# Kernel tuning notes

Measured on AMD Instinct MI355X. Metric: run time of the kernel, lower is better.

The kernel has to match this reference:

```python
import jax, jax.numpy as jnp
import numpy as np

D = 512  # token_dim == hidden_dim
K = 65536  # number of trajectory tokens


def safe_normalize(v, eps=1e-6):
    n = jnp.linalg.norm(v, axis=-1, keepdims=True)
    ok = n > eps
    e1 = jnp.zeros_like(v).at[..., 0].set(1.0)
    return jnp.where(ok, v / jnp.maximum(n, eps), e1)


def rot6d_to_matrix(x, eps=1e-6):
    # x: (K, 6) -> R: (K, 3, 3), rows (a1, b2, a3)
    a1 = safe_normalize(x[..., 0:3], eps)
    a2 = x[..., 3:6]
    proj = jnp.sum(a1 * a2, axis=-1, keepdims=True) * a1
    b2 = safe_normalize(a2 - proj, eps)
    a3 = safe_normalize(jnp.cross(a1, b2), eps)
    b2 = safe_normalize(jnp.cross(a3, a1), eps)
    return jnp.stack((a1, b2, a3), axis=-2)


def geodesic_angle(R_pred, R_gt, eps=1e-8):
    # RtR = R_gt^T @ R_pred, per-element (K,3,3)
    RtR = jnp.einsum('kji,kjl->kil', R_gt, R_pred)
    trace = RtR[..., 0, 0] + RtR[..., 1, 1] + RtR[..., 2, 2]
    c = jnp.clip((trace - 1.0) * 0.5, -1.0 + 1e-6, 1.0 - 1e-6)
    skew = RtR - jnp.swapaxes(RtR, -1, -2)
    v = jnp.stack([skew[..., 2, 1], skew[..., 0, 2], skew[..., 1, 0]], axis=-1)
    s = 0.5 * jnp.linalg.norm(v, axis=-1) + eps
    return jnp.arctan2(s, c)


def huber(pred, target, beta, mask):
    # smooth-L1 with beta, masked mean (denominator = clamped mask sum)
    d = jnp.abs(pred - target)
    l = jnp.where(d < beta, 0.5 * d * d / beta, d - 0.5 * beta) * mask
    return l.sum() / jnp.maximum(mask.sum(), 1.0)


def rot_loss_fn(pred, gt):
    # pred, gt: (K, 12) = [L rot6d(6), R rot6d(6)]
    Lp, Rp = pred[:, :6], pred[:, 6:]
    Lt, Rt = gt[:, :6], gt[:, 6:]
    Lvalid = jnp.all(Lt != -1000.0, axis=-1)
    Rvalid = jnp.all(Rt != -1000.0, axis=-1)
    safe6 = jnp.array([1.0, 0.0, 0.0, 0.0, 1.0, 0.0], pred.dtype)
    Lt = jnp.where(Lvalid[:, None], Lt, safe6)
    Rt = jnp.where(Rvalid[:, None], Rt, safe6)
    ang_L = geodesic_angle(rot6d_to_matrix(Lp), rot6d_to_matrix(Lt))
    ang_R = geodesic_angle(rot6d_to_matrix(Rp), rot6d_to_matrix(Rt))
    wL = Lvalid.astype(pred.dtype)
    wR = Rvalid.astype(pred.dtype)
    denom = jnp.maximum(wL.sum() + wR.sum(), 1e-8)
    num = jnp.sum(wL * jnp.where(Lvalid, ang_L, 0.0)) + jnp.sum(wR * jnp.where(Rvalid, ang_R, 0.0))
    return num / denom


def _heads(hidden_states, w1, b1, w2, b2, w3, b3):
    # 4 stacked MLPs (m = time, coord, coord2d, quat), torch Linear layout (out, in)
    h1 = jax.nn.relu(jnp.einsum('kc,mhc->mkh', hidden_states, w1) + b1[:, None, :])
    h2 = jax.nn.relu(jnp.einsum('mkh,mgh->mkg', h1, w2) + b2[:, None, :])
    pred_time = h2[0] @ w3[0:1].T + b3[0:1]      # (K, 1)
    pred_coords = h2[1] @ w3[1:7].T + b3[1:7]    # (K, 6)
    pred_2d = h2[2] @ w3[7:11].T + b3[7:11]      # (K, 4)
    pred_quat = h2[3] @ w3[11:23].T + b3[11:23]  # (K, 12)
    return pred_time, pred_coords, pred_2d, pred_quat


def _loss(pred_time, pred_coords, pred_2d, pred_quat, gt,
          beta_3d=0.07, beta_2d=0.02, beta_time=3.0, sigma_time=3.0):
    time_gt = gt[:, 0:1]
    time_valid = (time_gt != -1000.0).astype(jnp.float32)
    xyz_gt = gt[:, 1:7]
    xyz_valid = (xyz_gt != -1000.0).astype(jnp.float32)
    uv_gt = gt[:, 7:11]
    uv_valid = (uv_gt != -1000.0).astype(jnp.float32)
    quat_gt = gt[:, 11:23]
    quat_valid = (quat_gt != -1000.0).astype(jnp.float32)

    time_loss = huber(pred_time, time_gt, beta_time, time_valid)

    dt = jnp.abs(pred_time - time_gt)
    w_t = jnp.where(time_valid.sum() > 0,
                    jnp.exp(-0.5 * (dt / sigma_time) ** 2) * time_valid,
                    jnp.ones_like(pred_time))  # (K, 1), broadcasts over feature dims

    loss_3d = huber(pred_coords, xyz_gt, beta_3d, xyz_valid * w_t)
    loss_2d = huber(pred_2d / 1408.0, uv_gt / 1408.0, beta_2d, uv_valid * w_t)
    quat_huber = huber(pred_quat, quat_gt, 0.2, quat_valid * w_t)
    rot_l = 0.15 * rot_loss_fn(pred_quat, quat_gt)

    return 1.0 * time_loss + 2.0 * loss_3d + 0.5 * loss_2d + 0.5 * quat_huber + rot_l


def setup_inputs() -> dict:
    key = jax.random.key(0)
    ks = jax.random.split(key, 6)
    s = 1.0 / np.sqrt(D)
    return {
        'hidden_states': jax.random.normal(ks[0], (K, D), jnp.float32),
        'gt_traj': jax.random.uniform(ks[1], (K, 23), jnp.float32),
        'w1': jax.random.normal(ks[2], (4, D, D), jnp.float32) * s,
        'b1': jnp.zeros((4, D), jnp.float32),
        'w2': jax.random.normal(ks[3], (4, D, D), jnp.float32) * s,
        'b2': jnp.zeros((4, D), jnp.float32),
        'w3': jax.random.normal(ks[4], (23, D), jnp.float32) * s,
        'b3': jnp.zeros((23,), jnp.float32),
    }


def reference(hidden_states, gt_traj, w1, b1, w2, b2, w3, b3):
    pred_time, pred_coords, pred_2d, pred_quat = _heads(hidden_states, w1, b1, w2, b2, w3, b3)
    total_loss = _loss(pred_time, pred_coords, pred_2d, pred_quat, gt_traj)
    packed = jnp.concatenate(
        [pred_coords.reshape(-1, 2, 3), pred_quat.reshape(-1, 2, 6)], axis=-1
    ).reshape(-1, 18)
    return pred_time, packed, total_loss
```

## Files before the change

kernel.cpp:

```cpp
#include <hip/hip_runtime.h>
#include <math.h>


#define KROWS 65536
#define DH 512

typedef _Float16 f16;
typedef _Float16 half8 __attribute__((ext_vector_type(8)));
typedef float floatx4 __attribute__((ext_vector_type(4)));

#define WS_WF16   0
#define WS_W3F16  4194304
#define WS_PRED2D 4227072
#define WS_PART   5275648

__global__ __launch_bounds__(256) void convert_weights(
    const float* __restrict__ w1, const float* __restrict__ w2,
    const float* __restrict__ w3, f16* __restrict__ wf16, f16* __restrict__ w3f16)
{
  int t = blockIdx.x * 256 + threadIdx.x;
  if (t < 262144) {
    int ml = t >> 15;
    int mm = ml >> 1, l = ml & 1;
    int r = t & 32767;
    int fb = r >> 6;
    int lane = r & 63;
    int nt = fb >> 4, kq = fb & 15;
    int n = nt * 16 + (lane & 15);
    int k = kq * 32 + (lane >> 4) * 8;
    const float* src = (l ? w2 : w1) + (size_t)mm * 262144 + n * 512 + k;
    floatx4 u0 = *(const floatx4*)(src);
    floatx4 u1 = *(const floatx4*)(src + 4);
    half8 h;
    h[0] = (f16)u0[0]; h[1] = (f16)u0[1]; h[2] = (f16)u0[2]; h[3] = (f16)u0[3];
    h[4] = (f16)u1[0]; h[5] = (f16)u1[1]; h[6] = (f16)u1[2]; h[7] = (f16)u1[3];
    *(half8*)(wf16 + (size_t)ml * 262144 + fb * 512 + lane * 8) = h;
  } else {
    int j = t - 262144;
    if (j < 23 * DH) w3f16[j] = (f16)w3[j];
  }
}

extern __shared__ unsigned char smem[];

__global__ __launch_bounds__(512, 2) void fused_kernel(
    const float* __restrict__ hidden,
    const f16* __restrict__ wf16,
    const f16* __restrict__ w3f16,
    const float* __restrict__ b1g,
    const float* __restrict__ b2g,
    const float* __restrict__ b3g,
    float* __restrict__ dout,
    float* __restrict__ pred2d)
{
  const int r0  = blockIdx.x * 64;
  const int tid = threadIdx.x;
  const int w   = __builtin_amdgcn_readfirstlane(tid >> 6);
  const int lane = tid & 63;
  const int l15 = lane & 15;
  const int lg  = lane >> 4;

  unsigned char* Ab = smem;
  unsigned char* hb = smem + 65536;

  const int arow = l15 * 128;
  const int ao   = (lg * 16) ^ ((l15 & 7) << 4);
  auto aread = [&](const unsigned char* chunk, int mt, int kq) -> half8 {
    return *(const half8*)(chunk + mt * 2048 + arow + (ao ^ (kq << 6)));
  };
  const f16* bptr = wf16 + lane * 8;
  auto bload = [&](int mm, int l, int g, int nt) -> half8 {
    return *(const half8*)(bptr + ((mm * 2 + l)) * 262144
                           + ((w * 4 + nt) * 16 + g) * 512);
  };

  {
    const int row = tid >> 3;
    const int cg  = tid & 7;
    const int sw  = ((cg * 16) ^ ((row & 7) << 4));
    const float* hr = hidden + (size_t)(r0 + row) * DH + cg * 8;
    unsigned char* dst = Ab + row * 128 + sw;
#pragma unroll
    for (int kc = 0; kc < 8; ++kc) {
      floatx4 u0 = *(const floatx4*)(hr + kc * 64);
      floatx4 u1 = *(const floatx4*)(hr + kc * 64 + 4);
      half8 p;
      p[0] = (f16)u0[0]; p[1] = (f16)u0[1]; p[2] = (f16)u0[2]; p[3] = (f16)u0[3];
      p[4] = (f16)u1[0]; p[5] = (f16)u1[1]; p[6] = (f16)u1[2]; p[7] = (f16)u1[3];
      *(half8*)(dst + kc * 8192) = p;
    }
  }

  floatx4 acc[4][4];
  const floatx4 zf = {0.f, 0.f, 0.f, 0.f};
  const half8 hz = {(f16)0, (f16)0, (f16)0, (f16)0, (f16)0, (f16)0, (f16)0, (f16)0};

  __syncthreads();

#pragma unroll 1
  for (int m = 0; m < 4; ++m) {
#pragma unroll
    for (int mt = 0; mt < 4; ++mt)
#pragma unroll
      for (int nt = 0; nt < 4; ++nt) acc[mt][nt] = zf;

    half8 c0 = bload(m, 0, 0, 0), c1 = bload(m, 0, 0, 1),
          c2 = bload(m, 0, 0, 2), c3 = bload(m, 0, 0, 3);
#pragma unroll 1
    for (int g = 0; g < 16; ++g) {
      half8 n0, n1, n2, n3;
      if (g < 15) {
        n0 = bload(m, 0, g + 1, 0); n1 = bload(m, 0, g + 1, 1);
        n2 = bload(m, 0, g + 1, 2); n3 = bload(m, 0, g + 1, 3);
      }
      const unsigned char* chunk = Ab + (g >> 1) * 8192;
#pragma unroll
      for (int mt = 0; mt < 4; ++mt) {
        half8 a = aread(chunk, mt, g & 1);
        acc[mt][0] = __builtin_amdgcn_mfma_f32_16x16x32_f16(a, c0, acc[mt][0], 0, 0, 0);
        acc[mt][1] = __builtin_amdgcn_mfma_f32_16x16x32_f16(a, c1, acc[mt][1], 0, 0, 0);
        acc[mt][2] = __builtin_amdgcn_mfma_f32_16x16x32_f16(a, c2, acc[mt][2], 0, 0, 0);
        acc[mt][3] = __builtin_amdgcn_mfma_f32_16x16x32_f16(a, c3, acc[mt][3], 0, 0, 0);
      }
      c0 = n0; c1 = n1; c2 = n2; c3 = n3;
    }

    {
      unsigned char* myc = hb + w * 8192;
#pragma unroll
      for (int nt = 0; nt < 4; ++nt) {
        const float bv = b1g[m * DH + w * 64 + nt * 16 + l15];
        const int cb = 2 * (nt * 16 + l15);
#pragma unroll
        for (int mt = 0; mt < 4; ++mt)
#pragma unroll
          for (int j = 0; j < 4; ++j) {
            float v = fmaxf(acc[mt][nt][j] + bv, 0.f);
            int row = mt * 16 + 4 * lg + j;
            *(f16*)(myc + row * 128 + (cb ^ ((row & 7) << 4))) = (f16)v;
          }
      }
    }
    __syncthreads();

#pragma unroll
    for (int mt = 0; mt < 4; ++mt)
#pragma unroll
      for (int nt = 0; nt < 4; ++nt) acc[mt][nt] = zf;

    c0 = bload(m, 1, 0, 0); c1 = bload(m, 1, 0, 1);
    c2 = bload(m, 1, 0, 2); c3 = bload(m, 1, 0, 3);
#pragma unroll 1
    for (int g = 0; g < 16; ++g) {
      half8 n0, n1, n2, n3;
      if (g < 15) {
        n0 = bload(m, 1, g + 1, 0); n1 = bload(m, 1, g + 1, 1);
        n2 = bload(m, 1, g + 1, 2); n3 = bload(m, 1, g + 1, 3);
      }
      const unsigned char* chunk = hb + (g >> 1) * 8192;
#pragma unroll
      for (int mt = 0; mt < 4; ++mt) {
        half8 a = aread(chunk, mt, g & 1);
        acc[mt][0] = __builtin_amdgcn_mfma_f32_16x16x32_f16(a, c0, acc[mt][0], 0, 0, 0);
        acc[mt][1] = __builtin_amdgcn_mfma_f32_16x16x32_f16(a, c1, acc[mt][1], 0, 0, 0);
        acc[mt][2] = __builtin_amdgcn_mfma_f32_16x16x32_f16(a, c2, acc[mt][2], 0, 0, 0);
        acc[mt][3] = __builtin_amdgcn_mfma_f32_16x16x32_f16(a, c3, acc[mt][3], 0, 0, 0);
      }
      c0 = n0; c1 = n1; c2 = n2; c3 = n3;
    }
    __syncthreads();

    {
      unsigned char* myc = hb + w * 8192;
#pragma unroll
      for (int nt = 0; nt < 4; ++nt) {
        const float bv = b2g[m * DH + w * 64 + nt * 16 + l15];
        const int cb = 2 * (nt * 16 + l15);
#pragma unroll
        for (int mt = 0; mt < 4; ++mt)
#pragma unroll
          for (int j = 0; j < 4; ++j) {
            float v = fmaxf(acc[mt][nt][j] + bv, 0.f);
            int row = mt * 16 + 4 * lg + j;
            *(f16*)(myc + row * 128 + (cb ^ ((row & 7) << 4))) = (f16)v;
          }
      }
    }
    __syncthreads();

    if (w < 4) {
      const int base_m = (m == 0) ? 0 : (m == 1) ? 1 : (m == 2) ? 7 : 11;
      const int cnt_m  = (m == 0) ? 1 : (m == 1) ? 6 : (m == 2) ? 4 : 12;
      const bool ovalid = l15 < cnt_m;
      const f16* w3row = w3f16 + (size_t)(base_m + (ovalid ? l15 : 0)) * DH;
      floatx4 acc3 = zf;
#pragma unroll
      for (int q = 0; q < 16; ++q) {
        half8 ah = aread(hb + (q >> 1) * 8192, w, q & 1);
        half8 wv = ovalid ? *(const half8*)(w3row + q * 32 + lg * 8) : hz;
        acc3 = __builtin_amdgcn_mfma_f32_16x16x32_f16(ah, wv, acc3, 0, 0, 0);
      }
      if (ovalid) {
        const float bo = b3g[base_m + l15];
#pragma unroll
        for (int j = 0; j < 4; ++j) {
          const int row = r0 + w * 16 + 4 * lg + j;
          const float v = acc3[j] + bo;
          if (m == 0)      { if (l15 == 0) dout[row] = v; }
          else if (m == 1) { dout[KROWS + row * 18 + (l15 < 3 ? l15 : l15 + 6)] = v; }
          else if (m == 2) { pred2d[row * 4 + l15] = v; }
          else             { dout[KROWS + row * 18 + (l15 < 6 ? l15 + 3 : l15 + 6)] = v; }
        }
      }
    }
    __syncthreads();
  }
}

__device__ __forceinline__ void safe_norm3(float x, float y, float z, float* o) {
  float n = sqrtf(x * x + y * y + z * z);
  if (n > 1e-6f) { o[0] = x / n; o[1] = y / n; o[2] = z / n; }
  else           { o[0] = 1.f;   o[1] = 0.f;   o[2] = 0.f; }
}

__device__ __forceinline__ void rot6d(const float* x, float* R) {
  float a1[3]; safe_norm3(x[0], x[1], x[2], a1);
  float d = a1[0] * x[3] + a1[1] * x[4] + a1[2] * x[5];
  float b2[3]; safe_norm3(x[3] - d * a1[0], x[4] - d * a1[1], x[5] - d * a1[2], b2);
  float a3[3];
  safe_norm3(a1[1] * b2[2] - a1[2] * b2[1],
             a1[2] * b2[0] - a1[0] * b2[2],
             a1[0] * b2[1] - a1[1] * b2[0], a3);
  float bb[3];
  safe_norm3(a3[1] * a1[2] - a3[2] * a1[1],
             a3[2] * a1[0] - a3[0] * a1[2],
             a3[0] * a1[1] - a3[1] * a1[0], bb);
  R[0] = a1[0]; R[1] = a1[1]; R[2] = a1[2];
  R[3] = bb[0]; R[4] = bb[1]; R[5] = bb[2];
  R[6] = a3[0]; R[7] = a3[1]; R[8] = a3[2];
}

__device__ __forceinline__ float geo_angle(const float* P, const float* G) {
  float M[9];
#pragma unroll
  for (int i = 0; i < 3; ++i)
#pragma unroll
    for (int l = 0; l < 3; ++l)
      M[i * 3 + l] = G[0 + i] * P[0 + l] + G[3 + i] * P[3 + l] + G[6 + i] * P[6 + l];
  float tr = M[0] + M[4] + M[8];
  float c = fminf(fmaxf((tr - 1.f) * 0.5f, -1.f + 1e-6f), 1.f - 1e-6f);
  float v0 = M[7] - M[5], v1 = M[2] - M[6], v2 = M[3] - M[1];
  float s = 0.5f * sqrtf(v0 * v0 + v1 * v1 + v2 * v2) + 1e-8f;
  return atan2f(s, c);
}

__global__ __launch_bounds__(256) void loss_partial(
    const float* __restrict__ gt, const float* __restrict__ dout,
    const float* __restrict__ pred2d, float* __restrict__ partials)
{
  const int r = blockIdx.x * 256 + threadIdx.x;
  const float* g  = gt + (size_t)r * 23;
  const float* pk = dout + KROWS + (size_t)r * 18;
  float a[17];

  const float pt = dout[r];
  const float tg = g[0];
  const float tv = (tg != -1000.f) ? 1.f : 0.f;
  const float dt = fabsf(pt - tg);
  a[0] = ((dt < 3.f) ? (0.5f * dt * dt / 3.f) : (dt - 1.5f)) * tv;
  a[1] = tv;
  a[2] = tv;
  const float wt = expf(-0.5f * (dt / 3.f) * (dt / 3.f)) * tv;

  float n3T = 0.f, d3T = 0.f, n3F = 0.f, d3F = 0.f;
#pragma unroll
  for (int j = 0; j < 6; ++j) {
    const float p = pk[j < 3 ? j : j + 6];
    const float q = g[1 + j];
    const float val = (q != -1000.f) ? 1.f : 0.f;
    const float d = fabsf(p - q);
    const float l = (d < 0.07f) ? (0.5f * d * d / 0.07f) : (d - 0.035f);
    n3T += l * val * wt; d3T += val * wt; n3F += l * val; d3F += val;
  }
  a[3] = n3T; a[4] = d3T; a[5] = n3F; a[6] = d3F;

  float n2T = 0.f, d2T = 0.f, n2F = 0.f, d2F = 0.f;
#pragma unroll
  for (int j = 0; j < 4; ++j) {
    const float p = pred2d[(size_t)r * 4 + j];
    const float q = g[7 + j];
    const float val = (q != -1000.f) ? 1.f : 0.f;
    const float d = fabsf(p / 1408.f - q / 1408.f);
    const float l = (d < 0.02f) ? (0.5f * d * d / 0.02f) : (d - 0.01f);
    n2T += l * val * wt; d2T += val * wt; n2F += l * val; d2F += val;
  }
  a[7] = n2T; a[8] = d2T; a[9] = n2F; a[10] = d2F;

  float qp[12];
#pragma unroll
  for (int j = 0; j < 12; ++j) qp[j] = pk[j < 6 ? j + 3 : j + 6];
  float nqT = 0.f, dqT = 0.f, nqF = 0.f, dqF = 0.f;
#pragma unroll
  for (int j = 0; j < 12; ++j) {
    const float q = g[11 + j];
    const float val = (q != -1000.f) ? 1.f : 0.f;
    const float d = fabsf(qp[j] - q);
    const float l = (d < 0.2f) ? (0.5f * d * d / 0.2f) : (d - 0.1f);
    nqT += l * val * wt; dqT += val * wt; nqF += l * val; dqF += val;
  }
  a[11] = nqT; a[12] = dqT; a[13] = nqF; a[14] = dqF;

  bool Lv = true, Rv = true;
#pragma unroll
  for (int j = 0; j < 6; ++j) {
    if (g[11 + j] == -1000.f) Lv = false;
    if (g[17 + j] == -1000.f) Rv = false;
  }
  const float safe6[6] = {1.f, 0.f, 0.f, 0.f, 1.f, 0.f};
  float Lt[6], Rt[6];
#pragma unroll
  for (int j = 0; j < 6; ++j) {
    Lt[j] = Lv ? g[11 + j] : safe6[j];
    Rt[j] = Rv ? g[17 + j] : safe6[j];
  }
  float Rp[9], Rg[9];
  rot6d(qp, Rp);     rot6d(Lt, Rg);
  const float angL = geo_angle(Rp, Rg);
  rot6d(qp + 6, Rp); rot6d(Rt, Rg);
  const float angR = geo_angle(Rp, Rg);
  a[15] = (Lv ? angL : 0.f) + (Rv ? angR : 0.f);
  a[16] = (Lv ? 1.f : 0.f) + (Rv ? 1.f : 0.f);

#pragma unroll
  for (int i = 0; i < 17; ++i) {
    float v = a[i];
#pragma unroll
    for (int off = 32; off > 0; off >>= 1) v += __shfl_down(v, off, 64);
    a[i] = v;
  }
  __shared__ float red[4][17];
  if ((threadIdx.x & 63) == 0) {
    const int wv = threadIdx.x >> 6;
#pragma unroll
    for (int i = 0; i < 17; ++i) red[wv][i] = a[i];
  }
  __syncthreads();
  if (threadIdx.x < 17)
    partials[blockIdx.x * 20 + threadIdx.x] =
        red[0][threadIdx.x] + red[1][threadIdx.x] + red[2][threadIdx.x] + red[3][threadIdx.x];
}

__global__ void loss_final(const float* __restrict__ partials, float* __restrict__ dout)
{
  __shared__ float s[17];
  const int i = threadIdx.x;
  if (i < 17) {
    float v = 0.f;
    for (int b = 0; b < 256; ++b) v += partials[b * 20 + i];
    s[i] = v;
  }
  __syncthreads();
  if (i == 0) {
    const bool flag = s[2] > 0.f;
    const float time_loss = s[0] / fmaxf(s[1], 1.f);
    const float l3 = flag ? s[3] / fmaxf(s[4], 1.f) : s[5] / fmaxf(s[6], 1.f);
    const float l2 = flag ? s[7] / fmaxf(s[8], 1.f) : s[9] / fmaxf(s[10], 1.f);
    const float lq = flag ? s[11] / fmaxf(s[12], 1.f) : s[13] / fmaxf(s[14], 1.f);
    const float rot = 0.15f * (s[15] / fmaxf(s[16], 1e-8f));
    dout[19 * KROWS] = time_loss + 2.f * l3 + 0.5f * l2 + 0.5f * lq + rot;
  }
}

extern "C" void kernel_launch(void* const* d_in, const int* in_sizes, int n_in,
                              void* d_out, int out_size, void* d_ws, size_t ws_size,
                              hipStream_t stream) {
  (void)in_sizes; (void)n_in; (void)out_size; (void)ws_size;
  const float* hidden = (const float*)d_in[0];
  const float* gt     = (const float*)d_in[1];
  const float* w1     = (const float*)d_in[2];
  const float* b1     = (const float*)d_in[3];
  const float* w2     = (const float*)d_in[4];
  const float* b2     = (const float*)d_in[5];
  const float* w3     = (const float*)d_in[6];
  const float* b3     = (const float*)d_in[7];
  float* dout = (float*)d_out;

  unsigned char* ws = (unsigned char*)d_ws;
  f16*   wf16     = (f16*)(ws + WS_WF16);
  f16*   w3f16    = (f16*)(ws + WS_W3F16);
  float* pred2d   = (float*)(ws + WS_PRED2D);
  float* partials = (float*)(ws + WS_PART);

  static bool attr_done = false;
  if (!attr_done) {
    hipFuncSetAttribute(reinterpret_cast<const void*>(fused_kernel),
                        hipFuncAttributeMaxDynamicSharedMemorySize, 131072);
    attr_done = true;
  }

  convert_weights<<<1070, 256, 0, stream>>>(w1, w2, w3, wf16, w3f16);
  fused_kernel<<<1024, 512, 131072, stream>>>(hidden, wf16, w3f16, b1, b2, b3, dout, pred2d);
  loss_partial<<<256, 256, 0, stream>>>(gt, dout, pred2d, partials);
  loss_final<<<1, 64, 0, stream>>>(partials, dout);
}
```

Baseline: 370.6 us.

## Split fused MLP blocks into 32-row tiles and two head-pairs per block

Each block now handles 32 rows and only two of the four MLP heads, selected by block parity, so the grid grows to 4096 blocks. Shared memory per block drops to 64 KB and launch bounds request 4 blocks per CU, aiming for higher occupancy and better latency hiding. The cost is that every hidden row is loaded and converted twice, and each weight fragment feeds half as many MFMAs (2 row tiles instead of 4), which raises weight traffic per FLOP. A sync after the layer-1 GEMM replaces the end-of-loop sync so the layer-1 epilogue cannot overwrite hb while the previous head's output projection is still reading it.

```diff
diff --git a/kernel.cpp b/kernel.cpp
--- a/kernel.cpp
+++ b/kernel.cpp
@@ -43,7 +43,7 @@
 
 extern __shared__ unsigned char smem[];
 
-__global__ __launch_bounds__(512, 2) void fused_kernel(
+__global__ __launch_bounds__(512, 4) void fused_kernel(
     const float* __restrict__ hidden,
     const f16* __restrict__ wf16,
     const f16* __restrict__ w3f16,
@@ -53,7 +53,10 @@
     float* __restrict__ dout,
     float* __restrict__ pred2d)
 {
-  const int r0  = blockIdx.x * 64;
+  const int bid = blockIdx.x;
+  const int hp  = bid & 1;
+  const int row_tile = bid >> 1;
+  const int r0  = row_tile * 32;
   const int tid = threadIdx.x;
   const int w   = __builtin_amdgcn_readfirstlane(tid >> 6);
   const int lane = tid & 63;
@@ -61,12 +64,13 @@
   const int lg  = lane >> 4;
 
   unsigned char* Ab = smem;
-  unsigned char* hb = smem + 65536;
+  unsigned char* hb = smem + 32768;
 
   const int arow = l15 * 128;
   const int ao   = (lg * 16) ^ ((l15 & 7) << 4);
-  auto aread = [&](const unsigned char* chunk, int mt, int kq) -> half8 {
-    return *(const half8*)(chunk + mt * 2048 + arow + (ao ^ (kq << 6)));
+  auto aread = [&](const unsigned char* base, int g, int mt) -> half8 {
+    return *(const half8*)(base + (g >> 1) * 4096 + mt * 2048 + arow
+                           + (ao ^ ((g & 1) << 6)));
   };
   const f16* bptr = wf16 + lane * 8;
   auto bload = [&](int mm, int l, int g, int nt) -> half8 {
@@ -75,64 +79,69 @@
   };
 
   {
-    const int row = tid >> 3;
-    const int cg  = tid & 7;
-    const int sw  = ((cg * 16) ^ ((row & 7) << 4));
-    const float* hr = hidden + (size_t)(r0 + row) * DH + cg * 8;
-    unsigned char* dst = Ab + row * 128 + sw;
-#pragma unroll
-    for (int kc = 0; kc < 8; ++kc) {
-      floatx4 u0 = *(const floatx4*)(hr + kc * 64);
-      floatx4 u1 = *(const floatx4*)(hr + kc * 64 + 4);
-      half8 p;
-      p[0] = (f16)u0[0]; p[1] = (f16)u0[1]; p[2] = (f16)u0[2]; p[3] = (f16)u0[3];
-      p[4] = (f16)u1[0]; p[5] = (f16)u1[1]; p[6] = (f16)u1[2]; p[7] = (f16)u1[3];
-      *(half8*)(dst + kc * 8192) = p;
-    }
-  }
-
-  floatx4 acc[4][4];
+    const int row = tid >> 4;
+    const int cg  = tid & 15;
+    const float* hr = hidden + (size_t)(r0 + row) * DH;
+#pragma unroll
+    for (int p = 0; p < 4; ++p) {
+      const int col = p * 128 + cg * 8;
+      const int kc  = col >> 6;
+      const int cic = col & 63;
+      floatx4 u0 = *(const floatx4*)(hr + col);
+      floatx4 u1 = *(const floatx4*)(hr + col + 4);
+      half8 pk;
+      pk[0] = (f16)u0[0]; pk[1] = (f16)u0[1]; pk[2] = (f16)u0[2]; pk[3] = (f16)u0[3];
+      pk[4] = (f16)u1[0]; pk[5] = (f16)u1[1]; pk[6] = (f16)u1[2]; pk[7] = (f16)u1[3];
+      *(half8*)(Ab + kc * 4096 + row * 128 + ((2 * cic) ^ ((row & 7) << 4))) = pk;
+    }
+  }
+
+  floatx4 acc[2][4];
   const floatx4 zf = {0.f, 0.f, 0.f, 0.f};
   const half8 hz = {(f16)0, (f16)0, (f16)0, (f16)0, (f16)0, (f16)0, (f16)0, (f16)0};
 
   __syncthreads();
 
 #pragma unroll 1
-  for (int m = 0; m < 4; ++m) {
-#pragma unroll
-    for (int mt = 0; mt < 4; ++mt)
+  for (int mi = 0; mi < 2; ++mi) {
+    const int m = hp * 2 + mi;
+#pragma unroll
+    for (int mt = 0; mt < 2; ++mt)
 #pragma unroll
       for (int nt = 0; nt < 4; ++nt) acc[mt][nt] = zf;
 
-    half8 c0 = bload(m, 0, 0, 0), c1 = bload(m, 0, 0, 1),
-          c2 = bload(m, 0, 0, 2), c3 = bload(m, 0, 0, 3);
+    {
+      half8 c0 = bload(m, 0, 0, 0), c1 = bload(m, 0, 0, 1),
+            c2 = bload(m, 0, 0, 2), c3 = bload(m, 0, 0, 3);
 #pragma unroll 1
-    for (int g = 0; g < 16; ++g) {
-      half8 n0, n1, n2, n3;
-      if (g < 15) {
-        n0 = bload(m, 0, g + 1, 0); n1 = bload(m, 0, g + 1, 1);
-        n2 = bload(m, 0, g + 1, 2); n3 = bload(m, 0, g + 1, 3);
-      }
-      const unsigned char* chunk = Ab + (g >> 1) * 8192;
-#pragma unroll
-      for (int mt = 0; mt < 4; ++mt) {
-        half8 a = aread(chunk, mt, g & 1);
-        acc[mt][0] = __builtin_amdgcn_mfma_f32_16x16x32_f16(a, c0, acc[mt][0], 0, 0, 0);
-        acc[mt][1] = __builtin_amdgcn_mfma_f32_16x16x32_f16(a, c1, acc[mt][1], 0, 0, 0);
-        acc[mt][2] = __builtin_amdgcn_mfma_f32_16x16x32_f16(a, c2, acc[mt][2], 0, 0, 0);
-        acc[mt][3] = __builtin_amdgcn_mfma_f32_16x16x32_f16(a, c3, acc[mt][3], 0, 0, 0);
-      }
-      c0 = n0; c1 = n1; c2 = n2; c3 = n3;
-    }
+      for (int g = 0; g < 16; ++g) {
+        half8 n0, n1, n2, n3;
+        if (g < 15) {
+          n0 = bload(m, 0, g + 1, 0); n1 = bload(m, 0, g + 1, 1);
+          n2 = bload(m, 0, g + 1, 2); n3 = bload(m, 0, g + 1, 3);
+        }
+#pragma unroll
+        for (int mt = 0; mt < 2; ++mt) {
+          half8 a = aread(Ab, g, mt);
+          acc[mt][0] = __builtin_amdgcn_mfma_f32_16x16x32_f16(a, c0, acc[mt][0], 0, 0, 0);
+          acc[mt][1] = __builtin_amdgcn_mfma_f32_16x16x32_f16(a, c1, acc[mt][1], 0, 0, 0);
+          acc[mt][2] = __builtin_amdgcn_mfma_f32_16x16x32_f16(a, c2, acc[mt][2], 0, 0, 0);
+          acc[mt][3] = __builtin_amdgcn_mfma_f32_16x16x32_f16(a, c3, acc[mt][3], 0, 0, 0);
+        }
+        c0 = n0; c1 = n1; c2 = n2; c3 = n3;
+      }
+    }
+
+    __syncthreads();
 
     {
-      unsigned char* myc = hb + w * 8192;
+      unsigned char* myc = hb + w * 4096;
 #pragma unroll
       for (int nt = 0; nt < 4; ++nt) {
         const float bv = b1g[m * DH + w * 64 + nt * 16 + l15];
         const int cb = 2 * (nt * 16 + l15);
 #pragma unroll
-        for (int mt = 0; mt < 4; ++mt)
+        for (int mt = 0; mt < 2; ++mt)
 #pragma unroll
           for (int j = 0; j < 4; ++j) {
             float v = fmaxf(acc[mt][nt][j] + bv, 0.f);
@@ -144,40 +153,41 @@
     __syncthreads();
 
 #pragma unroll
-    for (int mt = 0; mt < 4; ++mt)
+    for (int mt = 0; mt < 2; ++mt)
 #pragma unroll
       for (int nt = 0; nt < 4; ++nt) acc[mt][nt] = zf;
 
-    c0 = bload(m, 1, 0, 0); c1 = bload(m, 1, 0, 1);
-    c2 = bload(m, 1, 0, 2); c3 = bload(m, 1, 0, 3);
+    {
+      half8 c0 = bload(m, 1, 0, 0), c1 = bload(m, 1, 0, 1),
+            c2 = bload(m, 1, 0, 2), c3 = bload(m, 1, 0, 3);
 #pragma unroll 1
-    for (int g = 0; g < 16; ++g) {
-      half8 n0, n1, n2, n3;
-      if (g < 15) {
-        n0 = bload(m, 1, g + 1, 0); n1 = bload(m, 1, g + 1, 1);
-        n2 = bload(m, 1, g + 1, 2); n3 = bload(m, 1, g + 1, 3);
-      }
-      const unsigned char* chunk = hb + (g >> 1) * 8192;
-#pragma unroll
-      for (int mt = 0; mt < 4; ++mt) {
-        half8 a = aread(chunk, mt, g & 1);
-        acc[mt][0] = __builtin_amdgcn_mfma_f32_16x16x32_f16(a, c0, acc[mt][0], 0, 0, 0);
-        acc[mt][1] = __builtin_amdgcn_mfma_f32_16x16x32_f16(a, c1, acc[mt][1], 0, 0, 0);
-        acc[mt][2] = __builtin_amdgcn_mfma_f32_16x16x32_f16(a, c2, acc[mt][2], 0, 0, 0);
-        acc[mt][3] = __builtin_amdgcn_mfma_f32_16x16x32_f16(a, c3, acc[mt][3], 0, 0, 0);
-      }
-      c0 = n0; c1 = n1; c2 = n2; c3 = n3;
+      for (int g = 0; g < 16; ++g) {
+        half8 n0, n1, n2, n3;
+        if (g < 15) {
+          n0 = bload(m, 1, g + 1, 0); n1 = bload(m, 1, g + 1, 1);
+          n2 = bload(m, 1, g + 1, 2); n3 = bload(m, 1, g + 1, 3);
+        }
+#pragma unroll
+        for (int mt = 0; mt < 2; ++mt) {
+          half8 a = aread(hb, g, mt);
+          acc[mt][0] = __builtin_amdgcn_mfma_f32_16x16x32_f16(a, c0, acc[mt][0], 0, 0, 0);
+          acc[mt][1] = __builtin_amdgcn_mfma_f32_16x16x32_f16(a, c1, acc[mt][1], 0, 0, 0);
+          acc[mt][2] = __builtin_amdgcn_mfma_f32_16x16x32_f16(a, c2, acc[mt][2], 0, 0, 0);
+          acc[mt][3] = __builtin_amdgcn_mfma_f32_16x16x32_f16(a, c3, acc[mt][3], 0, 0, 0);
+        }
+        c0 = n0; c1 = n1; c2 = n2; c3 = n3;
+      }
     }
     __syncthreads();
 
     {
-      unsigned char* myc = hb + w * 8192;
+      unsigned char* myc = hb + w * 4096;
 #pragma unroll
       for (int nt = 0; nt < 4; ++nt) {
         const float bv = b2g[m * DH + w * 64 + nt * 16 + l15];
         const int cb = 2 * (nt * 16 + l15);
 #pragma unroll
-        for (int mt = 0; mt < 4; ++mt)
+        for (int mt = 0; mt < 2; ++mt)
 #pragma unroll
           for (int j = 0; j < 4; ++j) {
             float v = fmaxf(acc[mt][nt][j] + bv, 0.f);
@@ -188,15 +198,15 @@
     }
     __syncthreads();
 
-    if (w < 4) {
+    if (w < 2) {
       const int base_m = (m == 0) ? 0 : (m == 1) ? 1 : (m == 2) ? 7 : 11;
       const int cnt_m  = (m == 0) ? 1 : (m == 1) ? 6 : (m == 2) ? 4 : 12;
       const bool ovalid = l15 < cnt_m;
       const f16* w3row = w3f16 + (size_t)(base_m + (ovalid ? l15 : 0)) * DH;
       floatx4 acc3 = zf;
-#pragma unroll
+#pragma unroll 2
       for (int q = 0; q < 16; ++q) {
-        half8 ah = aread(hb + (q >> 1) * 8192, w, q & 1);
+        half8 ah = aread(hb, q, w);
         half8 wv = ovalid ? *(const half8*)(w3row + q * 32 + lg * 8) : hz;
         acc3 = __builtin_amdgcn_mfma_f32_16x16x32_f16(ah, wv, acc3, 0, 0, 0);
       }
@@ -213,7 +223,6 @@
         }
       }
     }
-    __syncthreads();
   }
 }
 
@@ -394,12 +403,12 @@
   static bool attr_done = false;
   if (!attr_done) {
     hipFuncSetAttribute(reinterpret_cast<const void*>(fused_kernel),
-                        hipFuncAttributeMaxDynamicSharedMemorySize, 131072);
+                        hipFuncAttributeMaxDynamicSharedMemorySize, 65536);
     attr_done = true;
   }
 
   convert_weights<<<1070, 256, 0, stream>>>(w1, w2, w3, wf16, w3f16);
-  fused_kernel<<<1024, 512, 131072, stream>>>(hidden, wf16, w3f16, b1, b2, b3, dout, pred2d);
+  fused_kernel<<<4096, 512, 65536, stream>>>(hidden, wf16, w3f16, b1, b2, b3, dout, pred2d);
   loss_partial<<<256, 256, 0, stream>>>(gt, dout, pred2d, partials);
   loss_final<<<1, 64, 0, stream>>>(partials, dout);
 }
```

New measurement: 458.1 us. 23.6% more time.

## Split the four MLP heads across blocks and reuse one shared buffer in place

Applied to the files above, without the earlier changes.

Each block now handles one head for one 64-row tile, so the grid grows from 1024 to 4096 blocks. Blocks with the same row tile are interleaved in launch order so they run close together. LDS per block drops from 128KB dynamic to 64KB static by writing hidden activations back over the input buffer. Launch bounds now request four waves per EU for higher occupancy. In exchange, each hidden tile is loaded and converted four times instead of once, and register pressure is tighter under the new occupancy target.

```diff
diff --git a/kernel.cpp b/kernel.cpp
--- a/kernel.cpp
+++ b/kernel.cpp
@@ -41,9 +41,9 @@
   }
 }
 
-extern __shared__ unsigned char smem[];
-
-__global__ __launch_bounds__(512, 2) void fused_kernel(
+__global__ __launch_bounds__(512, 4)
+__attribute__((amdgpu_waves_per_eu(4, 4)))
+void fused_kernel(
     const float* __restrict__ hidden,
     const f16* __restrict__ wf16,
     const f16* __restrict__ w3f16,
@@ -53,25 +53,28 @@
     float* __restrict__ dout,
     float* __restrict__ pred2d)
 {
-  const int r0  = blockIdx.x * 64;
+  __shared__ __align__(16) unsigned char smem[65536];
+
+  const int bid = blockIdx.x;
+  const int rr  = bid & 7;
+  const int m   = rr >> 1;
+  const int row_tile = ((bid >> 3) << 1) | (rr & 1);
+  const int r0  = row_tile * 64;
   const int tid = threadIdx.x;
   const int w   = __builtin_amdgcn_readfirstlane(tid >> 6);
   const int lane = tid & 63;
   const int l15 = lane & 15;
   const int lg  = lane >> 4;
 
-  unsigned char* Ab = smem;
-  unsigned char* hb = smem + 65536;
-
   const int arow = l15 * 128;
   const int ao   = (lg * 16) ^ ((l15 & 7) << 4);
-  auto aread = [&](const unsigned char* chunk, int mt, int kq) -> half8 {
-    return *(const half8*)(chunk + mt * 2048 + arow + (ao ^ (kq << 6)));
+  auto aread = [&](int g, int mt) -> half8 {
+    return *(const half8*)(smem + (g >> 1) * 8192 + mt * 2048 + arow
+                           + (ao ^ ((g & 1) << 6)));
   };
-  const f16* bptr = wf16 + lane * 8;
-  auto bload = [&](int mm, int l, int g, int nt) -> half8 {
-    return *(const half8*)(bptr + ((mm * 2 + l)) * 262144
-                           + ((w * 4 + nt) * 16 + g) * 512);
+  const f16* bptr = wf16 + (size_t)(m * 2) * 262144 + lane * 8;
+  auto bload = [&](int l, int g, int nt) -> half8 {
+    return *(const half8*)(bptr + l * 262144 + ((w * 4 + nt) * 16 + g) * 512);
   };
 
   {
@@ -79,7 +82,7 @@
     const int cg  = tid & 7;
     const int sw  = ((cg * 16) ^ ((row & 7) << 4));
     const float* hr = hidden + (size_t)(r0 + row) * DH + cg * 8;
-    unsigned char* dst = Ab + row * 128 + sw;
+    unsigned char* dst = smem + row * 128 + sw;
 #pragma unroll
     for (int kc = 0; kc < 8; ++kc) {
       floatx4 u0 = *(const floatx4*)(hr + kc * 64);
@@ -97,26 +100,24 @@
 
   __syncthreads();
 
-#pragma unroll 1
-  for (int m = 0; m < 4; ++m) {
-#pragma unroll
-    for (int mt = 0; mt < 4; ++mt)
-#pragma unroll
-      for (int nt = 0; nt < 4; ++nt) acc[mt][nt] = zf;
-
-    half8 c0 = bload(m, 0, 0, 0), c1 = bload(m, 0, 0, 1),
-          c2 = bload(m, 0, 0, 2), c3 = bload(m, 0, 0, 3);
+#pragma unroll
+  for (int mt = 0; mt < 4; ++mt)
+#pragma unroll
+    for (int nt = 0; nt < 4; ++nt) acc[mt][nt] = zf;
+
+  {
+    half8 c0 = bload(0, 0, 0), c1 = bload(0, 0, 1),
+          c2 = bload(0, 0, 2), c3 = bload(0, 0, 3);
 #pragma unroll 1
     for (int g = 0; g < 16; ++g) {
       half8 n0, n1, n2, n3;
       if (g < 15) {
-        n0 = bload(m, 0, g + 1, 0); n1 = bload(m, 0, g + 1, 1);
-        n2 = bload(m, 0, g + 1, 2); n3 = bload(m, 0, g + 1, 3);
+        n0 = bload(0, g + 1, 0); n1 = bload(0, g + 1, 1);
+        n2 = bload(0, g + 1, 2); n3 = bload(0, g + 1, 3);
       }
-      const unsigned char* chunk = Ab + (g >> 1) * 8192;
 #pragma unroll
       for (int mt = 0; mt < 4; ++mt) {
-        half8 a = aread(chunk, mt, g & 1);
+        half8 a = aread(g, mt);
         acc[mt][0] = __builtin_amdgcn_mfma_f32_16x16x32_f16(a, c0, acc[mt][0], 0, 0, 0);
         acc[mt][1] = __builtin_amdgcn_mfma_f32_16x16x32_f16(a, c1, acc[mt][1], 0, 0, 0);
         acc[mt][2] = __builtin_amdgcn_mfma_f32_16x16x32_f16(a, c2, acc[mt][2], 0, 0, 0);
@@ -124,43 +125,46 @@
       }
       c0 = n0; c1 = n1; c2 = n2; c3 = n3;
     }
-
-    {
-      unsigned char* myc = hb + w * 8192;
-#pragma unroll
-      for (int nt = 0; nt < 4; ++nt) {
-        const float bv = b1g[m * DH + w * 64 + nt * 16 + l15];
-        const int cb = 2 * (nt * 16 + l15);
-#pragma unroll
-        for (int mt = 0; mt < 4; ++mt)
-#pragma unroll
-          for (int j = 0; j < 4; ++j) {
-            float v = fmaxf(acc[mt][nt][j] + bv, 0.f);
-            int row = mt * 16 + 4 * lg + j;
-            *(f16*)(myc + row * 128 + (cb ^ ((row & 7) << 4))) = (f16)v;
-          }
-      }
-    }
-    __syncthreads();
-
-#pragma unroll
-    for (int mt = 0; mt < 4; ++mt)
-#pragma unroll
-      for (int nt = 0; nt < 4; ++nt) acc[mt][nt] = zf;
-
-    c0 = bload(m, 1, 0, 0); c1 = bload(m, 1, 0, 1);
-    c2 = bload(m, 1, 0, 2); c3 = bload(m, 1, 0, 3);
+  }
+
+  __syncthreads();
+
+  {
+    unsigned char* myc = smem + w * 8192;
+#pragma unroll
+    for (int nt = 0; nt < 4; ++nt) {
+      const float bv = b1g[m * DH + w * 64 + nt * 16 + l15];
+      const int cb = 2 * (nt * 16 + l15);
+#pragma unroll
+      for (int mt = 0; mt < 4; ++mt)
+#pragma unroll
+        for (int j = 0; j < 4; ++j) {
+          float v = fmaxf(acc[mt][nt][j] + bv, 0.f);
+          int row = mt * 16 + 4 * lg + j;
+          *(f16*)(myc + row * 128 + (cb ^ ((row & 7) << 4))) = (f16)v;
+        }
+    }
+  }
+  __syncthreads();
+
+#pragma unroll
+  for (int mt = 0; mt < 4; ++mt)
+#pragma unroll
+    for (int nt = 0; nt < 4; ++nt) acc[mt][nt] = zf;
+
+  {
+    half8 c0 = bload(1, 0, 0), c1 = bload(1, 0, 1),
+          c2 = bload(1, 0, 2), c3 = bload(1, 0, 3);
 #pragma unroll 1
     for (int g = 0; g < 16; ++g) {
       half8 n0, n1, n2, n3;
       if (g < 15) {
-        n0 = bload(m, 1, g + 1, 0); n1 = bload(m, 1, g + 1, 1);
-        n2 = bload(m, 1, g + 1, 2); n3 = bload(m, 1, g + 1, 3);
+        n0 = bload(1, g + 1, 0); n1 = bload(1, g + 1, 1);
+        n2 = bload(1, g + 1, 2); n3 = bload(1, g + 1, 3);
       }
-      const unsigned char* chunk = hb + (g >> 1) * 8192;
 #pragma unroll
       for (int mt = 0; mt < 4; ++mt) {
-        half8 a = aread(chunk, mt, g & 1);
+        half8 a = aread(g, mt);
         acc[mt][0] = __builtin_amdgcn_mfma_f32_16x16x32_f16(a, c0, acc[mt][0], 0, 0, 0);
         acc[mt][1] = __builtin_amdgcn_mfma_f32_16x16x32_f16(a, c1, acc[mt][1], 0, 0, 0);
         acc[mt][2] = __builtin_amdgcn_mfma_f32_16x16x32_f16(a, c2, acc[mt][2], 0, 0, 0);
@@ -168,52 +172,52 @@
       }
       c0 = n0; c1 = n1; c2 = n2; c3 = n3;
     }
-    __syncthreads();
-
-    {
-      unsigned char* myc = hb + w * 8192;
-#pragma unroll
-      for (int nt = 0; nt < 4; ++nt) {
-        const float bv = b2g[m * DH + w * 64 + nt * 16 + l15];
-        const int cb = 2 * (nt * 16 + l15);
-#pragma unroll
-        for (int mt = 0; mt < 4; ++mt)
-#pragma unroll
-          for (int j = 0; j < 4; ++j) {
-            float v = fmaxf(acc[mt][nt][j] + bv, 0.f);
-            int row = mt * 16 + 4 * lg + j;
-            *(f16*)(myc + row * 128 + (cb ^ ((row & 7) << 4))) = (f16)v;
-          }
+  }
+
+  __syncthreads();
+
+  {
+    unsigned char* myc = smem + w * 8192;
+#pragma unroll
+    for (int nt = 0; nt < 4; ++nt) {
+      const float bv = b2g[m * DH + w * 64 + nt * 16 + l15];
+      const int cb = 2 * (nt * 16 + l15);
+#pragma unroll
+      for (int mt = 0; mt < 4; ++mt)
+#pragma unroll
+        for (int j = 0; j < 4; ++j) {
+          float v = fmaxf(acc[mt][nt][j] + bv, 0.f);
+          int row = mt * 16 + 4 * lg + j;
+          *(f16*)(myc + row * 128 + (cb ^ ((row & 7) << 4))) = (f16)v;
+        }
+    }
+  }
+  __syncthreads();
+
+  if (w < 4) {
+    const int base_m = (m == 0) ? 0 : (m == 1) ? 1 : (m == 2) ? 7 : 11;
+    const int cnt_m  = (m == 0) ? 1 : (m == 1) ? 6 : (m == 2) ? 4 : 12;
+    const bool ovalid = l15 < cnt_m;
+    const f16* w3row = w3f16 + (size_t)(base_m + (ovalid ? l15 : 0)) * DH;
+    floatx4 acc3 = zf;
+#pragma unroll 2
+    for (int q = 0; q < 16; ++q) {
+      half8 ah = aread(q, w);
+      half8 wv = ovalid ? *(const half8*)(w3row + q * 32 + lg * 8) : hz;
+      acc3 = __builtin_amdgcn_mfma_f32_16x16x32_f16(ah, wv, acc3, 0, 0, 0);
+    }
+    if (ovalid) {
+      const float bo = b3g[base_m + l15];
+#pragma unroll
+      for (int j = 0; j < 4; ++j) {
+        const int row = r0 + w * 16 + 4 * lg + j;
+        const float v = acc3[j] + bo;
+        if (m == 0)      { if (l15 == 0) dout[row] = v; }
+        else if (m == 1) { dout[KROWS + row * 18 + (l15 < 3 ? l15 : l15 + 6)] = v; }
+        else if (m == 2) { pred2d[row * 4 + l15] = v; }
+        else             { dout[KROWS + row * 18 + (l15 < 6 ? l15 + 3 : l15 + 6)] = v; }
       }
     }
-    __syncthreads();
-
-    if (w < 4) {
-      const int base_m = (m == 0) ? 0 : (m == 1) ? 1 : (m == 2) ? 7 : 11;
-      const int cnt_m  = (m == 0) ? 1 : (m == 1) ? 6 : (m == 2) ? 4 : 12;
-      const bool ovalid = l15 < cnt_m;
-      const f16* w3row = w3f16 + (size_t)(base_m + (ovalid ? l15 : 0)) * DH;
-      floatx4 acc3 = zf;
-#pragma unroll
-      for (int q = 0; q < 16; ++q) {
-        half8 ah = aread(hb + (q >> 1) * 8192, w, q & 1);
-        half8 wv = ovalid ? *(const half8*)(w3row + q * 32 + lg * 8) : hz;
-        acc3 = __builtin_amdgcn_mfma_f32_16x16x32_f16(ah, wv, acc3, 0, 0, 0);
-      }
-      if (ovalid) {
-        const float bo = b3g[base_m + l15];
-#pragma unroll
-        for (int j = 0; j < 4; ++j) {
-          const int row = r0 + w * 16 + 4 * lg + j;
-          const float v = acc3[j] + bo;
-          if (m == 0)      { if (l15 == 0) dout[row] = v; }
-          else if (m == 1) { dout[KROWS + row * 18 + (l15 < 3 ? l15 : l15 + 6)] = v; }
-          else if (m == 2) { pred2d[row * 4 + l15] = v; }
-          else             { dout[KROWS + row * 18 + (l15 < 6 ? l15 + 3 : l15 + 6)] = v; }
-        }
-      }
-    }
-    __syncthreads();
   }
 }
 
@@ -391,15 +395,8 @@
   float* pred2d   = (float*)(ws + WS_PRED2D);
   float* partials = (float*)(ws + WS_PART);
 
-  static bool attr_done = false;
-  if (!attr_done) {
-    hipFuncSetAttribute(reinterpret_cast<const void*>(fused_kernel),
-                        hipFuncAttributeMaxDynamicSharedMemorySize, 131072);
-    attr_done = true;
-  }
-
   convert_weights<<<1070, 256, 0, stream>>>(w1, w2, w3, wf16, w3f16);
-  fused_kernel<<<1024, 512, 131072, stream>>>(hidden, wf16, w3f16, b1, b2, b3, dout, pred2d);
+  fused_kernel<<<4096, 512, 0, stream>>>(hidden, wf16, w3f16, b1, b2, b3, dout, pred2d);
   loss_partial<<<256, 256, 0, stream>>>(gt, dout, pred2d, partials);
   loss_final<<<1, 64, 0, stream>>>(partials, dout);
 }
```

Measured after the change: 396.7 us. 1.07x slower.
